# Performance work log

Hardware: AMD Instinct MI355X
Metric: run time of the kernel (lower is better)

Reference implementation:

```python
import jax, jax.numpy as jnp
import numpy as np

B, NP, P, DIM = 128, 64, 128, 512
DST, DCONV, DEPTH = 16, 4, 2
DIN = 2 * DIM          # expand * dim
DTR = DIM // 16        # dt_rank
NCLS = 32


def setup_inputs() -> dict:
    key = jax.random.key(0)
    ks = jax.random.split(key, 12)
    r = lambda k, shape, s=0.02: jax.random.normal(k, shape, jnp.float32) * s
    A_log = jnp.log(jnp.arange(1, DST + 1, dtype=jnp.float32))  # S4D-real init
    return {
        "series": jax.random.normal(ks[0], (B, NP * P), jnp.float32),
        "seg_w": r(ks[1], (NP, P, DIM)),
        "seg_b": jnp.zeros((NP, DIM), jnp.float32),
        "ln_g": jnp.ones((NP, DIM), jnp.float32),
        "ln_b": jnp.zeros((NP, DIM), jnp.float32),
        "in_proj_w": r(ks[2], (DEPTH, 2 * DIN, DIM)),
        "conv_w": r(ks[3], (DEPTH, DIN, DCONV), 0.1),
        "conv_b": jnp.zeros((DEPTH, DIN), jnp.float32),
        "x_proj_w": r(ks[4], (DEPTH, DTR + 2 * DST, DIN)),
        "dt_proj_w": r(ks[5], (DEPTH, DIN, DTR), 0.1),
        "dt_proj_b": r(ks[6], (DEPTH, DIN), 0.5) - 4.0,  # small softplus(dt)
        "A_log": jnp.tile(A_log, (DEPTH, DIN, 1)),
        "D": jnp.ones((DEPTH, DIN), jnp.float32),
        "out_proj_w": r(ks[7], (DEPTH, DIM, DIN)),
        "head_ln_g": jnp.ones((NP * DIM,), jnp.float32),
        "head_ln_b": jnp.zeros((NP * DIM,), jnp.float32),
        "head_w": r(ks[8], (NCLS, NP * DIM)),
        "head_b": jnp.zeros((NCLS,), jnp.float32),
    }


def _layernorm(x, g, b, eps=1e-5):
    mu = x.mean(-1, keepdims=True)
    var = x.var(-1, keepdims=True)
    return (x - mu) / jnp.sqrt(var + eps) * g + b


def _mamba_block(x, wi, cw, cb, wx, wdt, bdt, A_log, Dp, wo):
    # x: [b, l, DIM]
    b, l, _ = x.shape
    xz = jnp.einsum('bld,ed->ble', x, wi)            # [b, l, 2*DIN]
    u, z = jnp.split(xz, 2, axis=-1)
    # depthwise causal conv1d (kernel DCONV, left pad DCONV-1)
    up = jnp.pad(u, ((0, 0), (DCONV - 1, 0), (0, 0)))
    uc = sum(up[:, k:k + l, :] * cw[:, k] for k in range(DCONV)) + cb
    uc = jax.nn.silu(uc)
    x_dbl = jnp.einsum('bld,ed->ble', uc, wx)        # [b, l, DTR+2*DST]
    dt, Bm, Cm = jnp.split(x_dbl, [DTR, DTR + DST], axis=-1)
    delta = jax.nn.softplus(jnp.einsum('blr,dr->bld', dt, wdt) + bdt)  # [b,l,DIN]
    A = -jnp.exp(A_log)                               # [DIN, DST]

    def step(h, inp):
        d_t, B_t, C_t, u_t = inp                      # [b,DIN],[b,DST],[b,DST],[b,DIN]
        dA = jnp.exp(d_t[:, :, None] * A)             # [b, DIN, DST]
        h = dA * h + (d_t * u_t)[:, :, None] * B_t[:, None, :]
        y = jnp.einsum('bdn,bn->bd', h, C_t)
        return h, y

    xs = (delta.transpose(1, 0, 2), Bm.transpose(1, 0, 2),
          Cm.transpose(1, 0, 2), uc.transpose(1, 0, 2))
    h0 = jnp.zeros((b, DIN, DST), x.dtype)
    _, ys = jax.lax.scan(step, h0, xs)                # [l, b, DIN]
    y = ys.transpose(1, 0, 2) + uc * Dp
    y = y * jax.nn.silu(z)
    return jnp.einsum('bld,ed->ble', y, wo)           # [b, l, DIM]


def _forward(series, seg_w, seg_b, ln_g, ln_b, in_proj_w, conv_w, conv_b,
             x_proj_w, dt_proj_w, dt_proj_b, A_log, D, out_proj_w,
             head_ln_g, head_ln_b, head_w, head_b):
    b = series.shape[0]
    x = series.reshape(b, NP, P)                      # equal-size pathway split
    x = jnp.einsum('bnp,npd->bnd', x, seg_w) + seg_b  # per-pathway Linear
    x = _layernorm(x, ln_g, ln_b)                     # per-pathway LayerNorm
    for i in range(DEPTH):                            # stacked Mamba (no residual)
        x = _mamba_block(x, in_proj_w[i], conv_w[i], conv_b[i], x_proj_w[i],
                         dt_proj_w[i], dt_proj_b[i], A_log[i], D[i], out_proj_w[i])
    x = x.reshape(b, NP * DIM)
    x = _layernorm(x, head_ln_g, head_ln_b)
    return x @ head_w.T + head_b


def reference(series, seg_w, seg_b, ln_g, ln_b, in_proj_w, conv_w, conv_b,
              x_proj_w, dt_proj_w, dt_proj_b, A_log, D, out_proj_w,
              head_ln_g, head_ln_b, head_w, head_b):
    return _forward(series, seg_w, seg_b, ln_g, ln_b, in_proj_w, conv_w, conv_b,
                    x_proj_w, dt_proj_w, dt_proj_b, A_log, D, out_proj_w,
                    head_ln_g, head_ln_b, head_w, head_b)
```

## Files before the change

### kernel.cpp

```cpp
#include <hip/hip_runtime.h>

typedef unsigned short u16;
typedef unsigned int   u32;
typedef __attribute__((ext_vector_type(8))) short short8;
typedef __attribute__((ext_vector_type(4))) float floatx4;

static __device__ __forceinline__ float silu_f(float x){
  return x / (1.f + __expf(-x));
}
static __device__ __forceinline__ float bfu2f(u16 u){
  union { u32 i; float f; } v; v.i = ((u32)u) << 16; return v.f;
}
static __device__ __forceinline__ u16 f2bfu(float f){
  union { float f; u32 i; } v; v.f = f;
  u32 x = v.i;
  u32 r = (x + 0x7fffu + ((x >> 16) & 1u)) >> 16;
  return (u16)r;
}
static __device__ __forceinline__ float softplus_f(float v){
  return fmaxf(v, 0.f) + log1pf(__expf(-fabsf(v)));
}

constexpr int cB = 128, cNP = 64, cP = 128, cDIM = 512, cDIN = 1024;
constexpr int cDST = 16, cDTR = 32, cNCLS = 32;
constexpr int cBL = cB * cNP;
constexpr int cXZ = 2 * cDIN;

__global__ __launch_bounds__(256) void k_f2bf(
    const float* __restrict__ src, u16* __restrict__ dst)
{
  const int i = (blockIdx.x * 256 + threadIdx.x) * 4;
  float4 v = *(const float4*)(src + i);
  ushort4 o;
  o.x = f2bfu(v.x); o.y = f2bfu(v.y); o.z = f2bfu(v.z); o.w = f2bfu(v.w);
  *(ushort4*)(dst + i) = o;
}

__global__ __launch_bounds__(256) void k_segT(
    const float* __restrict__ src, u16* __restrict__ dst)
{
  const int n = blockIdx.z;
  const int p0 = blockIdx.x * 32;
  const int d0 = blockIdx.y * 32;
  const int tx = threadIdx.x & 31;
  const int ty = threadIdx.x >> 5;
  __shared__ float t[32][33];
#pragma unroll
  for (int r = 0; r < 4; ++r)
    t[ty + r * 8][tx] = src[(size_t)n * (cP * cDIM) + (p0 + ty + r * 8) * cDIM + d0 + tx];
  __syncthreads();
#pragma unroll
  for (int r = 0; r < 4; ++r)
    dst[(size_t)n * (cDIM * cP) + (d0 + ty + r * 8) * cP + p0 + tx] =
        f2bfu(t[tx][ty + r * 8]);
}

template<bool AF32, int EPI>
__global__ __launch_bounds__(256) void k_gemm_mfma(
    const void* __restrict__ Av, int lda,
    const u16* __restrict__ W,
    float* __restrict__ C, int ldc,
    u16* __restrict__ Cb, int ldcb,
    const float* __restrict__ bias,
    int K, long azs, long wzs, long czs)
{
  constexpr int LDT = 40;
  __shared__ __align__(16) u16 As[128 * LDT];
  __shared__ __align__(16) u16 Ws[128 * LDT];

  const int bz = blockIdx.z;
  const u16* Wz = W + (size_t)bz * wzs;

  const int tid = threadIdx.x;
  const int bm = blockIdx.x * 128;
  const int bn = blockIdx.y * 128;
  const int wave = tid >> 6;
  const int lane = tid & 63;
  const int wm = (wave & 1) * 64;
  const int wn = (wave >> 1) * 64;
  const int l15 = lane & 15;
  const int quad = lane >> 4;

  floatx4 acc[4][4];
#pragma unroll
  for (int i = 0; i < 4; ++i)
#pragma unroll
    for (int j = 0; j < 4; ++j) acc[i][j] = (floatx4){0.f, 0.f, 0.f, 0.f};

  const int r0 = tid >> 2;
  const int c0 = (tid & 3) * 8;

  for (int k0 = 0; k0 < K; k0 += 32) {
    if constexpr (AF32) {
      const float* A = (const float*)Av + bz * azs;
#pragma unroll
      for (int h = 0; h < 2; ++h) {
        const float* p = A + (size_t)(bm + r0 + h * 64) * lda + k0 + c0;
        float4 va = *(const float4*)p;
        float4 vb = *(const float4*)(p + 4);
        short8 st;
        st[0] = (short)f2bfu(va.x); st[1] = (short)f2bfu(va.y);
        st[2] = (short)f2bfu(va.z); st[3] = (short)f2bfu(va.w);
        st[4] = (short)f2bfu(vb.x); st[5] = (short)f2bfu(vb.y);
        st[6] = (short)f2bfu(vb.z); st[7] = (short)f2bfu(vb.w);
        *(short8*)&As[(r0 + h * 64) * LDT + c0] = st;
      }
    } else {
      const u16* A = (const u16*)Av + bz * azs;
      short8 va0 = *(const short8*)(A + (size_t)(bm + r0)      * lda + k0 + c0);
      short8 va1 = *(const short8*)(A + (size_t)(bm + r0 + 64) * lda + k0 + c0);
      *(short8*)&As[r0 * LDT + c0] = va0;
      *(short8*)&As[(r0 + 64) * LDT + c0] = va1;
    }
    short8 vw0 = *(const short8*)(Wz + (size_t)(bn + r0)      * K + k0 + c0);
    short8 vw1 = *(const short8*)(Wz + (size_t)(bn + r0 + 64) * K + k0 + c0);
    *(short8*)&Ws[r0 * LDT + c0] = vw0;
    *(short8*)&Ws[(r0 + 64) * LDT + c0] = vw1;
    __syncthreads();

    short8 af[4], bf[4];
#pragma unroll
    for (int i = 0; i < 4; ++i)
      af[i] = *(const short8*)&As[(wm + i * 16 + l15) * LDT + quad * 8];
#pragma unroll
    for (int j = 0; j < 4; ++j)
      bf[j] = *(const short8*)&Ws[(wn + j * 16 + l15) * LDT + quad * 8];
#pragma unroll
    for (int i = 0; i < 4; ++i)
#pragma unroll
      for (int j = 0; j < 4; ++j)
        acc[i][j] = __builtin_amdgcn_mfma_f32_16x16x32_bf16(
            af[i], bf[j], acc[i][j], 0, 0, 0);
    __syncthreads();
  }

#pragma unroll
  for (int i = 0; i < 4; ++i) {
    const int m0 = bm + wm + i * 16 + quad * 4;
#pragma unroll
    for (int j = 0; j < 4; ++j) {
      const int n = bn + wn + j * 16 + l15;
      if constexpr (EPI == 1) {
        const float bs = bias[n];
#pragma unroll
        for (int r = 0; r < 4; ++r)
          C[(size_t)(m0 + r) * ldc + n + bz * czs] = softplus_f(acc[i][j][r] + bs);
      } else {
        if (C) {
#pragma unroll
          for (int r = 0; r < 4; ++r)
            C[(size_t)(m0 + r) * ldc + n + bz * czs] = acc[i][j][r];
        }
        if (Cb) {
#pragma unroll
          for (int r = 0; r < 4; ++r)
            Cb[(size_t)(m0 + r) * ldcb + n + bz * czs] = f2bfu(acc[i][j][r]);
        }
      }
    }
  }
}

__global__ __launch_bounds__(256) void k_ln(
    const float* __restrict__ xs, const float* __restrict__ sb,
    const float* __restrict__ ln_g, const float* __restrict__ ln_b,
    u16* __restrict__ x0b)
{
  const int tid = threadIdx.x;
  const int r = blockIdx.x * 4 + (tid >> 6);
  const int lane = tid & 63;
  const int d = lane * 8;
  const int n = r & 63;

  const float* row = xs + (size_t)r * cDIM + d;
  float4 a = *(const float4*)row;
  float4 b = *(const float4*)(row + 4);
  const float* sbp = sb + n * cDIM + d;
  float4 s0 = *(const float4*)sbp;
  float4 s1 = *(const float4*)(sbp + 4);
  a.x += s0.x; a.y += s0.y; a.z += s0.z; a.w += s0.w;
  b.x += s1.x; b.y += s1.y; b.z += s1.z; b.w += s1.w;

  float s  = a.x + a.y + a.z + a.w + b.x + b.y + b.z + b.w;
  float s2 = a.x*a.x + a.y*a.y + a.z*a.z + a.w*a.w
           + b.x*b.x + b.y*b.y + b.z*b.z + b.w*b.w;
#pragma unroll
  for (int m = 1; m < 64; m <<= 1) {
    s  += __shfl_xor(s,  m, 64);
    s2 += __shfl_xor(s2, m, 64);
  }
  const float mu = s * (1.f / cDIM);
  const float var = s2 * (1.f / cDIM) - mu * mu;
  const float rstd = rsqrtf(var + 1e-5f);

  const float* g = ln_g + n * cDIM + d;
  const float* be = ln_b + n * cDIM + d;
  float4 g0 = *(const float4*)g, g1 = *(const float4*)(g + 4);
  float4 b0 = *(const float4*)be, b1 = *(const float4*)(be + 4);
  ushort4 o0, o1;
  o0.x = f2bfu((a.x - mu) * rstd * g0.x + b0.x);
  o0.y = f2bfu((a.y - mu) * rstd * g0.y + b0.y);
  o0.z = f2bfu((a.z - mu) * rstd * g0.z + b0.z);
  o0.w = f2bfu((a.w - mu) * rstd * g0.w + b0.w);
  o1.x = f2bfu((b.x - mu) * rstd * g1.x + b1.x);
  o1.y = f2bfu((b.y - mu) * rstd * g1.y + b1.y);
  o1.z = f2bfu((b.z - mu) * rstd * g1.z + b1.z);
  o1.w = f2bfu((b.w - mu) * rstd * g1.w + b1.w);
  *(ushort4*)(x0b + (size_t)r * cDIM + d) = o0;
  *(ushort4*)(x0b + (size_t)r * cDIM + d + 4) = o1;
}

__global__ __launch_bounds__(256) void k_conv(
    const float* __restrict__ xz, const float* __restrict__ cw,
    const float* __restrict__ cb, u16* __restrict__ uc)
{
  const int t = blockIdx.x * 256 + threadIdx.x;
  const int b = t >> 10;
  const int d = t & 1023;
  const float w0 = cw[d * 4 + 0], w1 = cw[d * 4 + 1];
  const float w2 = cw[d * 4 + 2], w3 = cw[d * 4 + 3];
  const float bias = cb[d];
  const float* src = xz + (size_t)b * cNP * cXZ + d;
  u16* dst = uc + (size_t)b * cNP * cDIN + d;

  float u0 = 0.f, u1 = 0.f, u2 = 0.f;
  float cur[8];
#pragma unroll
  for (int i = 0; i < 8; ++i) cur[i] = src[(size_t)i * cXZ];

  for (int c = 0; c < 8; ++c) {
    float nxt[8];
    if (c < 7) {
#pragma unroll
      for (int i = 0; i < 8; ++i) nxt[i] = src[(size_t)((c + 1) * 8 + i) * cXZ];
    }
    u16 o[8];
#pragma unroll
    for (int i = 0; i < 8; ++i) {
      float v = w0 * u0 + w1 * u1 + w2 * u2 + w3 * cur[i] + bias;
      o[i] = f2bfu(silu_f(v));
      u0 = u1; u1 = u2; u2 = cur[i];
    }
#pragma unroll
    for (int i = 0; i < 8; ++i) dst[(size_t)(c * 8 + i) * cDIN] = o[i];
    if (c < 7) {
#pragma unroll
      for (int i = 0; i < 8; ++i) cur[i] = nxt[i];
    }
  }
}

__global__ __launch_bounds__(128) void k_xproj(
    const u16* __restrict__ A, const u16* __restrict__ W,
    float* __restrict__ xpart)
{
  constexpr int LDT = 40;
  __shared__ __align__(16) u16 As[128 * LDT];
  __shared__ __align__(16) u16 Ws[64 * LDT];

  const int tid = threadIdx.x;
  const int bm = blockIdx.x * 128;
  const int kbase = blockIdx.y * 256;
  const int wave = tid >> 6;
  const int lane = tid & 63;
  const int wm = wave * 64;
  const int l15 = lane & 15;
  const int quad = lane >> 4;

  floatx4 acc[4][4];
#pragma unroll
  for (int i = 0; i < 4; ++i)
#pragma unroll
    for (int j = 0; j < 4; ++j) acc[i][j] = (floatx4){0.f, 0.f, 0.f, 0.f};

  for (int kk = 0; kk < 256; kk += 32) {
    const int k0 = kbase + kk;
#pragma unroll
    for (int it = 0; it < 4; ++it) {
      int idx = tid + it * 128;
      int row = idx >> 2, c0 = (idx & 3) * 8;
      *(short8*)&As[row * LDT + c0] =
          *(const short8*)(A + (size_t)(bm + row) * cDIN + k0 + c0);
    }
#pragma unroll
    for (int it = 0; it < 2; ++it) {
      int idx = tid + it * 128;
      int row = idx >> 2, c0 = (idx & 3) * 8;
      *(short8*)&Ws[row * LDT + c0] =
          *(const short8*)(W + (size_t)row * cDIN + k0 + c0);
    }
    __syncthreads();

    short8 af[4], bf[4];
#pragma unroll
    for (int i = 0; i < 4; ++i)
      af[i] = *(const short8*)&As[(wm + i * 16 + l15) * LDT + quad * 8];
#pragma unroll
    for (int j = 0; j < 4; ++j)
      bf[j] = *(const short8*)&Ws[(j * 16 + l15) * LDT + quad * 8];
#pragma unroll
    for (int i = 0; i < 4; ++i)
#pragma unroll
      for (int j = 0; j < 4; ++j)
        acc[i][j] = __builtin_amdgcn_mfma_f32_16x16x32_bf16(
            af[i], bf[j], acc[i][j], 0, 0, 0);
    __syncthreads();
  }

  float* out = xpart + (size_t)blockIdx.y * cBL * 64;
#pragma unroll
  for (int i = 0; i < 4; ++i) {
    const int m0 = bm + wm + i * 16 + quad * 4;
#pragma unroll
    for (int j = 0; j < 4; ++j) {
      const int n = j * 16 + l15;
#pragma unroll
      for (int r = 0; r < 4; ++r)
        out[(size_t)(m0 + r) * 64 + n] = acc[i][j][r];
    }
  }
}

__global__ __launch_bounds__(256) void k_xred(
    const float* __restrict__ xpart, float* __restrict__ C,
    u16* __restrict__ Cb)
{
  const int i = (blockIdx.x * 256 + threadIdx.x) * 4;
  float4 s = *(const float4*)(xpart + i);
#pragma unroll
  for (int k = 1; k < 4; ++k) {
    float4 v = *(const float4*)(xpart + (size_t)k * cBL * 64 + i);
    s.x += v.x; s.y += v.y; s.z += v.z; s.w += v.w;
  }
  *(float4*)(C + i) = s;
  ushort4 o;
  o.x = f2bfu(s.x); o.y = f2bfu(s.y); o.z = f2bfu(s.z); o.w = f2bfu(s.w);
  *(ushort4*)(Cb + i) = o;
}

__global__ __launch_bounds__(256) void k_scan(
    const float* __restrict__ xz, u16* __restrict__ uc,
    const float* __restrict__ xdbl, const float* __restrict__ A_log,
    const float* __restrict__ Dp)
{
  const int b = blockIdx.x;
  const int tid = threadIdx.x;
  const int d = blockIdx.y * 256 + tid;

  __shared__ float sBC[cNP][32];
  {
    const float4* src = (const float4*)xdbl;
    for (int i = tid; i < cNP * 8; i += 256) {
      int l = i >> 3, q = i & 7;
      *(float4*)&sBC[l][q * 4] = src[(size_t)(b * cNP + l) * 16 + 8 + q];
    }
  }

  float A[cDST];
  {
    const float4* ap = (const float4*)(A_log + (size_t)d * cDST);
#pragma unroll
    for (int q = 0; q < 4; ++q) {
      float4 w = ap[q];
      A[q*4+0] = -__expf(w.x); A[q*4+1] = -__expf(w.y);
      A[q*4+2] = -__expf(w.z); A[q*4+3] = -__expf(w.w);
    }
  }
  float h[cDST];
#pragma unroll
  for (int n = 0; n < cDST; ++n) h[n] = 0.f;
  const float Dv = Dp[d];
  __syncthreads();

  const float* dsrc = xz + d;
  const float* zsrc = xz + cDIN + d;
  u16* usrc = uc + d;
  const size_t rb = (size_t)b * cNP;

  float dvc[8], zvc[8], uvc[8];
#pragma unroll
  for (int i = 0; i < 8; ++i) {
    dvc[i] = dsrc[(rb + i) * cXZ];
    zvc[i] = zsrc[(rb + i) * cXZ];
    uvc[i] = bfu2f(usrc[(rb + i) * cDIN]);
  }

  for (int c = 0; c < 8; ++c) {
    float dvn[8], zvn[8], uvn[8];
    if (c < 7) {
#pragma unroll
      for (int i = 0; i < 8; ++i) {
        const size_t row = rb + (c + 1) * 8 + i;
        dvn[i] = dsrc[row * cXZ];
        zvn[i] = zsrc[row * cXZ];
        uvn[i] = bfu2f(usrc[row * cDIN]);
      }
    }
    u16 yo[8];
#pragma unroll
    for (int i = 0; i < 8; ++i) {
      const int l = c * 8 + i;
      const float dv = dvc[i], zv = zvc[i], uv = uvc[i];
      const float du = dv * uv;
      float y = 0.f;
#pragma unroll
      for (int n = 0; n < cDST; ++n) {
        float dA = __expf(dv * A[n]);
        h[n] = dA * h[n] + du * sBC[l][n];
        y += h[n] * sBC[l][16 + n];
      }
      y = (y + uv * Dv) * silu_f(zv);
      yo[i] = f2bfu(y);
    }
#pragma unroll
    for (int i = 0; i < 8; ++i)
      usrc[(rb + c * 8 + i) * cDIN] = yo[i];
    if (c < 7) {
#pragma unroll
      for (int i = 0; i < 8; ++i) {
        dvc[i] = dvn[i]; zvc[i] = zvn[i]; uvc[i] = uvn[i];
      }
    }
  }
}

__global__ __launch_bounds__(256) void k_hstats1(
    const float* __restrict__ x, float* __restrict__ pst)
{
  const int b = blockIdx.x;
  const int chunk = blockIdx.y;
  const int tid = threadIdx.x;
  const float4* r4 = (const float4*)(x + (size_t)b * (cNP * cDIM) + chunk * 4096);
  float4 v = r4[tid];
  float4 w = r4[tid + 256];
  float4 u = r4[tid + 512];
  float4 t = r4[tid + 768];
  float s  = v.x + v.y + v.z + v.w + w.x + w.y + w.z + w.w
           + u.x + u.y + u.z + u.w + t.x + t.y + t.z + t.w;
  float s2 = v.x*v.x + v.y*v.y + v.z*v.z + v.w*v.w
           + w.x*w.x + w.y*w.y + w.z*w.z + w.w*w.w
           + u.x*u.x + u.y*u.y + u.z*u.z + u.w*u.w
           + t.x*t.x + t.y*t.y + t.z*t.z + t.w*t.w;
  __shared__ float red[512];
  red[tid] = s; red[256 + tid] = s2;
  __syncthreads();
  for (int st = 128; st > 0; st >>= 1) {
    if (tid < st) { red[tid] += red[tid + st]; red[256+tid] += red[256+tid+st]; }
    __syncthreads();
  }
  if (tid == 0) {
    pst[(b * 8 + chunk) * 2]     = red[0];
    pst[(b * 8 + chunk) * 2 + 1] = red[256];
  }
}

__global__ __launch_bounds__(128) void k_hstats2(
    const float* __restrict__ pst, float* __restrict__ stats)
{
  const int b = threadIdx.x;
  float s = 0.f, s2 = 0.f;
#pragma unroll
  for (int c = 0; c < 8; ++c) {
    s  += pst[(b * 8 + c) * 2];
    s2 += pst[(b * 8 + c) * 2 + 1];
  }
  const float mu = s * (1.f / (cNP * cDIM));
  const float var = s2 * (1.f / (cNP * cDIM)) - mu * mu;
  stats[2 * b]     = mu;
  stats[2 * b + 1] = rsqrtf(var + 1e-5f);
}

__global__ __launch_bounds__(256) void k_head1(
    const float* __restrict__ x, const float* __restrict__ stats,
    const float* __restrict__ hg, const float* __restrict__ hb,
    const u16* __restrict__ hwb, float* __restrict__ hpart)
{
  const int b = blockIdx.x;
  const int chunk = blockIdx.y;
  const int tid = threadIdx.x;
  const float mu = stats[2 * b], rstd = stats[2 * b + 1];
  const float* row = x + (size_t)b * (cNP * cDIM);
  const int k0 = chunk * 2048;

  float acc[cNCLS];
#pragma unroll
  for (int c = 0; c < cNCLS; ++c) acc[c] = 0.f;

#pragma unroll
  for (int it = 0; it < 4; ++it) {
    const int i0 = k0 + it * 512 + tid * 2;
    float xn0 = (row[i0]     - mu) * rstd * hg[i0]     + hb[i0];
    float xn1 = (row[i0 + 1] - mu) * rstd * hg[i0 + 1] + hb[i0 + 1];
#pragma unroll
    for (int c = 0; c < cNCLS; ++c) {
      u32 w2 = *(const u32*)(hwb + (size_t)c * (cNP * cDIM) + i0);
      acc[c] += xn0 * bfu2f((u16)(w2 & 0xffffu)) + xn1 * bfu2f((u16)(w2 >> 16));
    }
  }

  __shared__ float sred[cNCLS * 257];
#pragma unroll
  for (int c = 0; c < cNCLS; ++c) sred[c * 257 + tid] = acc[c];
  __syncthreads();
  if (tid < cNCLS * 8) {
    const int c = tid >> 3, p = tid & 7;
    float s = 0.f;
#pragma unroll
    for (int i = 0; i < 32; ++i) s += sred[c * 257 + p * 32 + i];
    s += __shfl_xor(s, 1, 64);
    s += __shfl_xor(s, 2, 64);
    s += __shfl_xor(s, 4, 64);
    if (p == 0) hpart[(size_t)(b * 16 + chunk) * cNCLS + c] = s;
  }
}

__global__ __launch_bounds__(64) void k_head2(
    const float* __restrict__ hpart, const float* __restrict__ hbias,
    float* __restrict__ out)
{
  const int b = blockIdx.x;
  const int c = threadIdx.x;
  if (c < cNCLS) {
    float s = 0.f;
#pragma unroll
    for (int k = 0; k < 16; ++k)
      s += hpart[(size_t)(b * 16 + k) * cNCLS + c];
    out[b * cNCLS + c] = s + hbias[c];
  }
}

extern "C" void kernel_launch(void* const* d_in, const int* in_sizes, int n_in,
                              void* d_out, int out_size, void* d_ws, size_t ws_size,
                              hipStream_t stream)
{
  (void)in_sizes; (void)n_in; (void)out_size; (void)ws_size;

  const float* series    = (const float*)d_in[0];
  const float* seg_w     = (const float*)d_in[1];
  const float* seg_b     = (const float*)d_in[2];
  const float* ln_g      = (const float*)d_in[3];
  const float* ln_b      = (const float*)d_in[4];
  const float* in_proj_w = (const float*)d_in[5];
  const float* conv_w    = (const float*)d_in[6];
  const float* conv_b    = (const float*)d_in[7];
  const float* x_proj_w  = (const float*)d_in[8];
  const float* dt_proj_w = (const float*)d_in[9];
  const float* dt_proj_b = (const float*)d_in[10];
  const float* A_log     = (const float*)d_in[11];
  const float* Dp        = (const float*)d_in[12];
  const float* out_proj_w= (const float*)d_in[13];
  const float* head_ln_g = (const float*)d_in[14];
  const float* head_ln_b = (const float*)d_in[15];
  const float* head_w    = (const float*)d_in[16];
  const float* head_b    = (const float*)d_in[17];

  float* ws     = (float*)d_ws;
  float* xz     = ws;
  float* xsegf  = xz;
  float* x0     = xz;
  float* xdbl   = xz + (size_t)cBL * cXZ;
  float* stats  = xdbl + (size_t)cBL * 64;
  float* pst    = stats + 256;
  float* hpart  = pst + 128 * 8 * 2;
  u16*   x0b    = (u16*)(hpart + 128 * 16 * 32);
  u16*   wib    = x0b + (size_t)cBL * cDIM;
  u16*   wob    = wib + (size_t)2 * (2*cDIN) * cDIM;
  u16*   wdtb   = wob + (size_t)2 * cDIM * cDIN;
  u16*   wxb    = wdtb + (size_t)2 * cDIN * cDTR;
  u16*   xdbl16 = wxb + (size_t)2 * 64 * cDIN;
  u16*   wsegT  = xdbl16 + (size_t)cBL * 64;
  u16*   ucb16  = wsegT + (size_t)cNP * cDIM * cP;
  u16*   hwb    = ucb16 + (size_t)cBL * cDIN;
  float* xpart  = (float*)x0b;

  k_f2bf<<<(2 * (2*cDIN) * cDIM) / 1024, 256, 0, stream>>>(in_proj_w, wib);
  k_f2bf<<<(2 * cDIM * cDIN) / 1024, 256, 0, stream>>>(out_proj_w, wob);
  k_f2bf<<<(2 * cDIN * cDTR) / 1024, 256, 0, stream>>>(dt_proj_w, wdtb);
  k_f2bf<<<(2 * 64 * cDIN) / 1024, 256, 0, stream>>>(x_proj_w, wxb);
  k_f2bf<<<(cNCLS * cNP * cDIM) / 1024, 256, 0, stream>>>(head_w, hwb);
  k_segT<<<dim3(cP/32, cDIM/32, cNP), 256, 0, stream>>>(seg_w, wsegT);

  k_gemm_mfma<true,0><<<dim3(1, cDIM/128, cNP), 256, 0, stream>>>(
      series, cNP * cP, wsegT, xsegf, cNP * cDIM, (u16*)nullptr, 0,
      nullptr, cP, (long)cP, (long)cDIM * cP, (long)cDIM);
  k_ln<<<cBL / 4, 256, 0, stream>>>(xsegf, seg_b, ln_g, ln_b, x0b);

  for (int dep = 0; dep < 2; ++dep) {
    const u16*   wi  = wib  + (size_t)dep * (2*cDIN) * cDIM;
    const u16*   wo  = wob  + (size_t)dep * cDIM * cDIN;
    const u16*   wdt = wdtb + (size_t)dep * cDIN * cDTR;
    const u16*   wx  = wxb  + (size_t)dep * 64 * cDIN;
    const float* cwd = conv_w     + (size_t)dep * cDIN * 4;
    const float* cbd = conv_b     + (size_t)dep * cDIN;
    const float* bdt = dt_proj_b  + (size_t)dep * cDIN;
    const float* Ald = A_log      + (size_t)dep * cDIN * cDST;
    const float* Dd  = Dp         + (size_t)dep * cDIN;

    k_gemm_mfma<false,0><<<dim3(cBL/128, (2*cDIN)/128), 256, 0, stream>>>(
        x0b, cDIM, wi, xz, cXZ, (u16*)nullptr, 0, nullptr, cDIM, 0, 0, 0);
    k_conv<<<(cB * cDIN) / 256, 256, 0, stream>>>(xz, cwd, cbd, ucb16);
    k_xproj<<<dim3(cBL / 128, 4), 128, 0, stream>>>(ucb16, wx, xpart);
    k_xred<<<(cBL * 64) / 1024, 256, 0, stream>>>(xpart, xdbl, xdbl16);
    k_gemm_mfma<false,1><<<dim3(cBL/128, cDIN/128), 256, 0, stream>>>(
        xdbl16, 64, wdt, xz, cXZ, (u16*)nullptr, 0, bdt, cDTR, 0, 0, 0);
    k_scan<<<dim3(cB, 4), 256, 0, stream>>>(xz, ucb16, xdbl, Ald, Dd);
    k_gemm_mfma<false,0><<<dim3(cBL/128, cDIM/128), 256, 0, stream>>>(
        ucb16, cDIN, wo,
        dep ? x0 : (float*)nullptr, cDIM,
        dep ? (u16*)nullptr : x0b, cDIM,
        nullptr, cDIN, 0, 0, 0);
  }

  k_hstats1<<<dim3(cB, 8), 256, 0, stream>>>(x0, pst);
  k_hstats2<<<1, 128, 0, stream>>>(pst, stats);
  k_head1<<<dim3(cB, 16), 256, 0, stream>>>(x0, stats, head_ln_g, head_ln_b,
                                            hwb, hpart);
  k_head2<<<cB, 64, 0, stream>>>(hpart, head_b, (float*)d_out);
}
```

Before: 474.0 us.

## Store xz intermediate in bf16 and register-prefetch next K tile in GEMMs

The in_proj and dt_proj GEMMs now write their outputs as bf16 into a new xz16 buffer instead of fp32, and conv and scan read bf16 and convert on load. This halves the bytes written and read for the largest intermediate tensor. Separately, the MFMA GEMM and x_proj kernels prefetch the next K tile's global loads into registers while the current tile is computed, overlapping global latency with math. The cost is lower precision for u, z and delta, plus higher register pressure.

Measured after the change: 438.6 us. -7.5%, faster.

```diff
diff --git a/kernel.cpp b/kernel.cpp
--- a/kernel.cpp
+++ b/kernel.cpp
@@ -90,33 +90,59 @@
   const int r0 = tid >> 2;
   const int c0 = (tid & 3) * 8;
 
+  const float* Af = (const float*)Av + (AF32 ? (size_t)bz * azs : 0);
+  const u16*   Ab = (const u16*)Av + (AF32 ? 0 : (size_t)bz * azs);
+
+  float4 fa0, fb0, fa1, fb1;
+  short8 ra0, ra1, rw0, rw1;
+
+  if constexpr (AF32) {
+    const float* p0 = Af + (size_t)(bm + r0) * lda + c0;
+    const float* p1 = Af + (size_t)(bm + r0 + 64) * lda + c0;
+    fa0 = *(const float4*)p0; fb0 = *(const float4*)(p0 + 4);
+    fa1 = *(const float4*)p1; fb1 = *(const float4*)(p1 + 4);
+  } else {
+    ra0 = *(const short8*)(Ab + (size_t)(bm + r0)      * lda + c0);
+    ra1 = *(const short8*)(Ab + (size_t)(bm + r0 + 64) * lda + c0);
+  }
+  rw0 = *(const short8*)(Wz + (size_t)(bn + r0)      * K + c0);
+  rw1 = *(const short8*)(Wz + (size_t)(bn + r0 + 64) * K + c0);
+
   for (int k0 = 0; k0 < K; k0 += 32) {
     if constexpr (AF32) {
-      const float* A = (const float*)Av + bz * azs;
-#pragma unroll
-      for (int h = 0; h < 2; ++h) {
-        const float* p = A + (size_t)(bm + r0 + h * 64) * lda + k0 + c0;
-        float4 va = *(const float4*)p;
-        float4 vb = *(const float4*)(p + 4);
-        short8 st;
-        st[0] = (short)f2bfu(va.x); st[1] = (short)f2bfu(va.y);
-        st[2] = (short)f2bfu(va.z); st[3] = (short)f2bfu(va.w);
-        st[4] = (short)f2bfu(vb.x); st[5] = (short)f2bfu(vb.y);
-        st[6] = (short)f2bfu(vb.z); st[7] = (short)f2bfu(vb.w);
-        *(short8*)&As[(r0 + h * 64) * LDT + c0] = st;
+      short8 s0, s1;
+      s0[0] = (short)f2bfu(fa0.x); s0[1] = (short)f2bfu(fa0.y);
+      s0[2] = (short)f2bfu(fa0.z); s0[3] = (short)f2bfu(fa0.w);
+      s0[4] = (short)f2bfu(fb0.x); s0[5] = (short)f2bfu(fb0.y);
+      s0[6] = (short)f2bfu(fb0.z); s0[7] = (short)f2bfu(fb0.w);
+      s1[0] = (short)f2bfu(fa1.x); s1[1] = (short)f2bfu(fa1.y);
+      s1[2] = (short)f2bfu(fa1.z); s1[3] = (short)f2bfu(fa1.w);
+      s1[4] = (short)f2bfu(fb1.x); s1[5] = (short)f2bfu(fb1.y);
+      s1[6] = (short)f2bfu(fb1.z); s1[7] = (short)f2bfu(fb1.w);
+      *(short8*)&As[r0 * LDT + c0] = s0;
+      *(short8*)&As[(r0 + 64) * LDT + c0] = s1;
+    } else {
+      *(short8*)&As[r0 * LDT + c0] = ra0;
+      *(short8*)&As[(r0 + 64) * LDT + c0] = ra1;
+    }
+    *(short8*)&Ws[r0 * LDT + c0] = rw0;
+    *(short8*)&Ws[(r0 + 64) * LDT + c0] = rw1;
+    __syncthreads();
+
+    const int kn = k0 + 32;
+    if (kn < K) {
+      if constexpr (AF32) {
+        const float* p0 = Af + (size_t)(bm + r0) * lda + kn + c0;
+        const float* p1 = Af + (size_t)(bm + r0 + 64) * lda + kn + c0;
+        fa0 = *(const float4*)p0; fb0 = *(const float4*)(p0 + 4);
+        fa1 = *(const float4*)p1; fb1 = *(const float4*)(p1 + 4);
+      } else {
+        ra0 = *(const short8*)(Ab + (size_t)(bm + r0)      * lda + kn + c0);
+        ra1 = *(const short8*)(Ab + (size_t)(bm + r0 + 64) * lda + kn + c0);
       }
-    } else {
-      const u16* A = (const u16*)Av + bz * azs;
-      short8 va0 = *(const short8*)(A + (size_t)(bm + r0)      * lda + k0 + c0);
-      short8 va1 = *(const short8*)(A + (size_t)(bm + r0 + 64) * lda + k0 + c0);
-      *(short8*)&As[r0 * LDT + c0] = va0;
-      *(short8*)&As[(r0 + 64) * LDT + c0] = va1;
-    }
-    short8 vw0 = *(const short8*)(Wz + (size_t)(bn + r0)      * K + k0 + c0);
-    short8 vw1 = *(const short8*)(Wz + (size_t)(bn + r0 + 64) * K + k0 + c0);
-    *(short8*)&Ws[r0 * LDT + c0] = vw0;
-    *(short8*)&Ws[(r0 + 64) * LDT + c0] = vw1;
-    __syncthreads();
+      rw0 = *(const short8*)(Wz + (size_t)(bn + r0)      * K + kn + c0);
+      rw1 = *(const short8*)(Wz + (size_t)(bn + r0 + 64) * K + kn + c0);
+    }
 
     short8 af[4], bf[4];
 #pragma unroll
@@ -144,7 +170,8 @@
         const float bs = bias[n];
 #pragma unroll
         for (int r = 0; r < 4; ++r)
-          C[(size_t)(m0 + r) * ldc + n + bz * czs] = softplus_f(acc[i][j][r] + bs);
+          Cb[(size_t)(m0 + r) * ldcb + n + bz * czs] =
+              f2bfu(softplus_f(acc[i][j][r] + bs));
       } else {
         if (C) {
 #pragma unroll
@@ -211,7 +238,7 @@
 }
 
 __global__ __launch_bounds__(256) void k_conv(
-    const float* __restrict__ xz, const float* __restrict__ cw,
+    const u16* __restrict__ xz16, const float* __restrict__ cw,
     const float* __restrict__ cb, u16* __restrict__ uc)
 {
   const int t = blockIdx.x * 256 + threadIdx.x;
@@ -220,19 +247,20 @@
   const float w0 = cw[d * 4 + 0], w1 = cw[d * 4 + 1];
   const float w2 = cw[d * 4 + 2], w3 = cw[d * 4 + 3];
   const float bias = cb[d];
-  const float* src = xz + (size_t)b * cNP * cXZ + d;
+  const u16* src = xz16 + (size_t)b * cNP * cXZ + d;
   u16* dst = uc + (size_t)b * cNP * cDIN + d;
 
   float u0 = 0.f, u1 = 0.f, u2 = 0.f;
   float cur[8];
 #pragma unroll
-  for (int i = 0; i < 8; ++i) cur[i] = src[(size_t)i * cXZ];
+  for (int i = 0; i < 8; ++i) cur[i] = bfu2f(src[(size_t)i * cXZ]);
 
   for (int c = 0; c < 8; ++c) {
     float nxt[8];
     if (c < 7) {
 #pragma unroll
-      for (int i = 0; i < 8; ++i) nxt[i] = src[(size_t)((c + 1) * 8 + i) * cXZ];
+      for (int i = 0; i < 8; ++i)
+        nxt[i] = bfu2f(src[(size_t)((c + 1) * 8 + i) * cXZ]);
     }
     u16 o[8];
 #pragma unroll
@@ -273,23 +301,44 @@
 #pragma unroll
     for (int j = 0; j < 4; ++j) acc[i][j] = (floatx4){0.f, 0.f, 0.f, 0.f};
 
+  short8 rA[4], rW[2];
+#pragma unroll
+  for (int it = 0; it < 4; ++it) {
+    int idx = tid + it * 128, row = idx >> 2, cc = (idx & 3) * 8;
+    rA[it] = *(const short8*)(A + (size_t)(bm + row) * cDIN + kbase + cc);
+  }
+#pragma unroll
+  for (int it = 0; it < 2; ++it) {
+    int idx = tid + it * 128, row = idx >> 2, cc = (idx & 3) * 8;
+    rW[it] = *(const short8*)(W + (size_t)row * cDIN + kbase + cc);
+  }
+
   for (int kk = 0; kk < 256; kk += 32) {
-    const int k0 = kbase + kk;
 #pragma unroll
     for (int it = 0; it < 4; ++it) {
-      int idx = tid + it * 128;
-      int row = idx >> 2, c0 = (idx & 3) * 8;
-      *(short8*)&As[row * LDT + c0] =
-          *(const short8*)(A + (size_t)(bm + row) * cDIN + k0 + c0);
+      int idx = tid + it * 128, row = idx >> 2, cc = (idx & 3) * 8;
+      *(short8*)&As[row * LDT + cc] = rA[it];
     }
 #pragma unroll
     for (int it = 0; it < 2; ++it) {
-      int idx = tid + it * 128;
-      int row = idx >> 2, c0 = (idx & 3) * 8;
-      *(short8*)&Ws[row * LDT + c0] =
-          *(const short8*)(W + (size_t)row * cDIN + k0 + c0);
+      int idx = tid + it * 128, row = idx >> 2, cc = (idx & 3) * 8;
+      *(short8*)&Ws[row * LDT + cc] = rW[it];
     }
     __syncthreads();
+
+    if (kk + 32 < 256) {
+      const int k0 = kbase + kk + 32;
+#pragma unroll
+      for (int it = 0; it < 4; ++it) {
+        int idx = tid + it * 128, row = idx >> 2, cc = (idx & 3) * 8;
+        rA[it] = *(const short8*)(A + (size_t)(bm + row) * cDIN + k0 + cc);
+      }
+#pragma unroll
+      for (int it = 0; it < 2; ++it) {
+        int idx = tid + it * 128, row = idx >> 2, cc = (idx & 3) * 8;
+        rW[it] = *(const short8*)(W + (size_t)row * cDIN + k0 + cc);
+      }
+    }
 
     short8 af[4], bf[4];
 #pragma unroll
@@ -339,7 +388,7 @@
 }
 
 __global__ __launch_bounds__(256) void k_scan(
-    const float* __restrict__ xz, u16* __restrict__ uc,
+    const u16* __restrict__ xz16, u16* __restrict__ uc,
     const float* __restrict__ xdbl, const float* __restrict__ A_log,
     const float* __restrict__ Dp)
 {
@@ -372,16 +421,16 @@
   const float Dv = Dp[d];
   __syncthreads();
 
-  const float* dsrc = xz + d;
-  const float* zsrc = xz + cDIN + d;
+  const u16* dsrc = xz16 + d;
+  const u16* zsrc = xz16 + cDIN + d;
   u16* usrc = uc + d;
   const size_t rb = (size_t)b * cNP;
 
   float dvc[8], zvc[8], uvc[8];
 #pragma unroll
   for (int i = 0; i < 8; ++i) {
-    dvc[i] = dsrc[(rb + i) * cXZ];
-    zvc[i] = zsrc[(rb + i) * cXZ];
+    dvc[i] = bfu2f(dsrc[(rb + i) * cXZ]);
+    zvc[i] = bfu2f(zsrc[(rb + i) * cXZ]);
     uvc[i] = bfu2f(usrc[(rb + i) * cDIN]);
   }
 
@@ -391,8 +440,8 @@
 #pragma unroll
       for (int i = 0; i < 8; ++i) {
         const size_t row = rb + (c + 1) * 8 + i;
-        dvn[i] = dsrc[row * cXZ];
-        zvn[i] = zsrc[row * cXZ];
+        dvn[i] = bfu2f(dsrc[row * cXZ]);
+        zvn[i] = bfu2f(zsrc[row * cXZ]);
         uvn[i] = bfu2f(usrc[row * cDIN]);
       }
     }
@@ -554,11 +603,10 @@
   const float* head_w    = (const float*)d_in[16];
   const float* head_b    = (const float*)d_in[17];
 
-  float* ws     = (float*)d_ws;
-  float* xz     = ws;
-  float* xsegf  = xz;
-  float* x0     = xz;
-  float* xdbl   = xz + (size_t)cBL * cXZ;
+  u16*   xz16   = (u16*)d_ws;
+  float* x0     = (float*)(xz16 + (size_t)cBL * cXZ);
+  float* xsegf  = x0;
+  float* xdbl   = x0 + (size_t)cBL * cDIM;
   float* stats  = xdbl + (size_t)cBL * 64;
   float* pst    = stats + 256;
   float* hpart  = pst + 128 * 8 * 2;
@@ -597,13 +645,13 @@
     const float* Dd  = Dp         + (size_t)dep * cDIN;
 
     k_gemm_mfma<false,0><<<dim3(cBL/128, (2*cDIN)/128), 256, 0, stream>>>(
-        x0b, cDIM, wi, xz, cXZ, (u16*)nullptr, 0, nullptr, cDIM, 0, 0, 0);
-    k_conv<<<(cB * cDIN) / 256, 256, 0, stream>>>(xz, cwd, cbd, ucb16);
+        x0b, cDIM, wi, (float*)nullptr, 0, xz16, cXZ, nullptr, cDIM, 0, 0, 0);
+    k_conv<<<(cB * cDIN) / 256, 256, 0, stream>>>(xz16, cwd, cbd, ucb16);
     k_xproj<<<dim3(cBL / 128, 4), 128, 0, stream>>>(ucb16, wx, xpart);
     k_xred<<<(cBL * 64) / 1024, 256, 0, stream>>>(xpart, xdbl, xdbl16);
     k_gemm_mfma<false,1><<<dim3(cBL/128, cDIN/128), 256, 0, stream>>>(
-        xdbl16, 64, wdt, xz, cXZ, (u16*)nullptr, 0, bdt, cDTR, 0, 0, 0);
-    k_scan<<<dim3(cB, 4), 256, 0, stream>>>(xz, ucb16, xdbl, Ald, Dd);
+        xdbl16, 64, wdt, (float*)nullptr, 0, xz16, cXZ, bdt, cDTR, 0, 0, 0);
+    k_scan<<<dim3(cB, 4), 256, 0, stream>>>(xz16, ucb16, xdbl, Ald, Dd);
     k_gemm_mfma<false,0><<<dim3(cBL/128, cDIM/128), 256, 0, stream>>>(
         ucb16, cDIN, wo,
         dep ? x0 : (float*)nullptr, cDIM,
```
